# Optimization experiments

Hardware: AMD Instinct MI355X
Metric: run time of the kernel (lower is better)

Reference implementation:

```python
import jax, jax.numpy as jnp
import numpy as np

E = 8          # num_experts
K = 2          # top-k experts per token
CAP_RATIO = 1.05


def setup_inputs() -> dict:
    key = jax.random.key(0)
    ks = jax.random.split(key, 4)
    B, S, D, H = 2, 2048, 1024, 4096
    x = jax.random.normal(ks[0], (B, S, D), jnp.float32)
    Wg = jax.random.normal(ks[1], (E, D), jnp.float32) * 0.02
    W1 = jax.random.normal(ks[2], (E, D, H), jnp.float32) * 0.02
    b1 = jnp.zeros((E, H), jnp.float32)
    W2 = jax.random.normal(ks[3], (E, H, D), jnp.float32) * 0.02
    b2 = jnp.zeros((E, D), jnp.float32)
    return {"x": x, "Wg": Wg, "W1": W1, "b1": b1, "W2": W2, "b2": b2}


def reference(x, Wg, W1, b1, W2, b2):
    # Eval-mode SparseMoE forward (no router noise, no aux-loss metrics).
    B, S, D = x.shape
    T = B * S
    xf = x.reshape(T, D)

    # --- router: softmax gates + top-k ---
    gates = jax.nn.softmax(xf @ Wg.T, axis=-1)          # [T, E]
    topw, topi = jax.lax.top_k(gates, K)                # [T, K]

    # --- capacity-limited dispatch (slot-major order, matching torch loop) ---
    C = int(round(K * T * CAP_RATIO / E))               # buffer capacity per expert
    e_ord = topi.T.reshape(-1)                          # [K*T] expert id per assignment
    tok_ord = jnp.tile(jnp.arange(T), K)                # [K*T] token id per assignment
    oh = jax.nn.one_hot(e_ord, E, dtype=jnp.int32)      # [K*T, E]
    cnt = jnp.take_along_axis(jnp.cumsum(oh, 0) - oh, e_ord[:, None], 1)[:, 0]
    within = cnt < C                                    # first C arrivals per expert accepted
    pos = jnp.where(within, cnt, C)                     # dropped tokens -> dummy slot C

    # scatter accepted tokens into per-expert buffers [E, C+1, D]
    x_disp = xf[tok_ord]
    buf = jnp.zeros((E, C + 1, D), xf.dtype).at[e_ord, pos].add(x_disp)[:, :C]

    # --- grouped expert MLP (Linear -> exact GELU -> Linear) ---
    h = jax.nn.gelu(jnp.einsum('ecd,edh->ech', buf, W1) + b1[:, None, :],
                    approximate=False)
    y = jnp.einsum('ech,ehd->ecd', h, W2) + b2[:, None, :]  # [E, C, D]

    # --- gather back and weighted combine ---
    y_ord = y[e_ord, jnp.minimum(pos, C - 1)] * within[:, None].astype(y.dtype)
    y_tk = y_ord.reshape(K, T, D).transpose(1, 0, 2)     # [T, K, D]
    cw = topw * within.reshape(K, T).T.astype(topw.dtype)
    out = jnp.einsum('tk,tkd->td', cw, y_tk)
    return out.reshape(B, S, D)
```

## Files before the change

### kernel.cpp

```cpp
#include <hip/hip_runtime.h>

typedef __attribute__((ext_vector_type(8))) __bf16 bf16x8;
typedef __attribute__((ext_vector_type(4))) float f32x4;

constexpr int T  = 4096;
constexpr int Dm = 1024;
constexpr int Hm = 4096;
constexpr int NE = 8;
constexpr int CAP = 1075;
constexpr int CP  = 1152;

static __device__ __forceinline__ unsigned short f2bf(float f) {
  unsigned int u = __float_as_uint(f);
  u += 0x7FFFu + ((u >> 16) & 1u);
  return (unsigned short)(u >> 16);
}
static __device__ __forceinline__ float bf2f(unsigned short u) {
  return __uint_as_float(((unsigned int)u) << 16);
}

static __device__ __forceinline__ void gload_lds16(const void* g, void* l) {
  __builtin_amdgcn_global_load_lds(
      (const __attribute__((address_space(1))) void*)g,
      (__attribute__((address_space(3))) void*)l, 16, 0, 0);
}


static __device__ __forceinline__ void transpose_body(
    float (*tile)[33], const float* __restrict__ W, unsigned short* __restrict__ Wt,
    int Kd, int N, int e, int n0, int k0) {
  const float* src = W + ((long long)e * Kd + k0) * N + n0;
  const int tid = threadIdx.x;
  const int r = tid >> 3;
  const int c4 = (tid & 7) * 4;
#pragma unroll
  for (int hh = 0; hh < 2; ++hh) {
    float4 v = *(const float4*)(src + (long long)(r + 32 * hh) * N + c4);
    tile[r + 32 * hh][c4] = v.x; tile[r + 32 * hh][c4 + 1] = v.y;
    tile[r + 32 * hh][c4 + 2] = v.z; tile[r + 32 * hh][c4 + 3] = v.w;
  }
  __syncthreads();
  const int n = tid >> 4;
  const int k4 = (tid & 15) * 4;
  unsigned short* dst = Wt + ((long long)e * N + n0) * Kd + k0;
#pragma unroll
  for (int hh = 0; hh < 2; ++hh) {
    int nn = n + 16 * hh;
    ushort4 o;
    o.x = f2bf(tile[k4][nn]);     o.y = f2bf(tile[k4 + 1][nn]);
    o.z = f2bf(tile[k4 + 2][nn]); o.w = f2bf(tile[k4 + 3][nn]);
    *(ushort4*)(dst + (long long)nn * Kd + k4) = o;
  }
}

static __device__ __forceinline__ void router_body(
    const float* __restrict__ x, const float* __restrict__ Wg,
    int* __restrict__ topi, float* __restrict__ topw, int blk) {
  int t = blk * 4 + (threadIdx.x >> 6);
  int lane = threadIdx.x & 63;
  const float* xr = x + (size_t)t * Dm;
  float acc[NE];
#pragma unroll
  for (int e = 0; e < NE; ++e) acc[e] = 0.f;
  for (int i = lane * 4; i < Dm; i += 256) {
    float4 xv = *(const float4*)(xr + i);
#pragma unroll
    for (int e = 0; e < NE; ++e) {
      float4 wv = *(const float4*)(Wg + e * Dm + i);
      acc[e] += xv.x * wv.x + xv.y * wv.y + xv.z * wv.z + xv.w * wv.w;
    }
  }
#pragma unroll
  for (int off = 32; off > 0; off >>= 1) {
#pragma unroll
    for (int e = 0; e < NE; ++e) acc[e] += __shfl_xor(acc[e], off, 64);
  }
  if (lane == 0) {
    float mx = acc[0];
#pragma unroll
    for (int e = 1; e < NE; ++e) mx = fmaxf(mx, acc[e]);
    float g[NE];
    float s = 0.f;
#pragma unroll
    for (int e = 0; e < NE; ++e) { g[e] = expf(acc[e] - mx); s += g[e]; }
    int i0 = 0; float v0 = g[0];
#pragma unroll
    for (int e = 1; e < NE; ++e) if (g[e] > v0) { v0 = g[e]; i0 = e; }
    int i1 = -1; float v1 = -1e30f;
#pragma unroll
    for (int e = 0; e < NE; ++e) {
      if (e == i0) continue;
      if (g[e] > v1) { v1 = g[e]; i1 = e; }
    }
    float inv = 1.f / s;
    topi[t * 2] = i0; topi[t * 2 + 1] = i1;
    topw[t * 2] = v0 * inv; topw[t * 2 + 1] = v1 * inv;
  }
}

static __device__ __forceinline__ void stage_tile(
    unsigned short* Al, unsigned short* Bl,
    const unsigned short* __restrict__ Ab, const unsigned short* __restrict__ Btb,
    int Kd, int kb, int wid, int srow, int sslot) {
#pragma unroll
  for (int j = 0; j < 4; ++j) {
    const int c = wid * 4 + j;
    const long long rowg = 8 * c + srow;
    gload_lds16(Ab  + rowg * Kd + kb + sslot * 8, &Al[c * 512]);
    gload_lds16(Btb + rowg * Kd + kb + sslot * 8, &Bl[c * 512]);
  }
}

static __device__ __forceinline__ void compute_tile(
    const unsigned short* Al, const unsigned short* Bl,
    int wr, int wc, int l15, int khi, int swz, f32x4 (&acc)[4][4]) {
#pragma unroll
  for (int kk = 0; kk < 2; ++kk) {
    bf16x8 af[4], bfv[4];
#pragma unroll
    for (int m = 0; m < 4; ++m)
      af[m] = *(const bf16x8*)&Al[(wr + m * 16 + l15) * 64 + (((kk * 4 + khi) ^ swz) << 3)];
#pragma unroll
    for (int n = 0; n < 4; ++n)
      bfv[n] = *(const bf16x8*)&Bl[(wc + n * 16 + l15) * 64 + (((kk * 4 + khi) ^ swz) << 3)];
#pragma unroll
    for (int m = 0; m < 4; ++m)
#pragma unroll
      for (int n = 0; n < 4; ++n)
        acc[m][n] = __builtin_amdgcn_mfma_f32_16x16x32_bf16(af[m], bfv[n], acc[m][n], 0, 0, 0);
  }
}

static __device__ __forceinline__ void gemm_mainloop_db(
    char* smem, const unsigned short* __restrict__ Ab,
    const unsigned short* __restrict__ Btb, int Kd, f32x4 (&acc)[4][4]) {
  unsigned short* A0 = (unsigned short*)smem;
  unsigned short* B0 = (unsigned short*)(smem + 16384);
  unsigned short* A1 = (unsigned short*)(smem + 32768);
  unsigned short* B1 = (unsigned short*)(smem + 49152);
  const int tid = threadIdx.x;
  const int lane = tid & 63;
  const int wid = tid >> 6;
  const int wr = (wid >> 1) * 64;
  const int wc = (wid & 1) * 64;
  const int l15 = lane & 15;
  const int khi = lane >> 4;
  const int swz = lane & 7;
  const int srow = lane >> 3;
  const int sslot = (lane & 7) ^ srow;

  const int nK = Kd >> 6;
  stage_tile(A0, B0, Ab, Btb, Kd, 0, wid, srow, sslot);
  int cur = 0;
  for (int kt = 0; kt < nK - 1; ++kt) {
    unsigned short* An = cur ? A0 : A1;
    unsigned short* Bn = cur ? B0 : B1;
    stage_tile(An, Bn, Ab, Btb, Kd, (kt + 1) << 6, wid, srow, sslot);
    asm volatile("s_waitcnt vmcnt(8)" ::: "memory");
    __builtin_amdgcn_s_barrier();
    unsigned short* Ac = cur ? A1 : A0;
    unsigned short* Bc = cur ? B1 : B0;
    compute_tile(Ac, Bc, wr, wc, l15, khi, swz, acc);
    __builtin_amdgcn_s_barrier();
    cur ^= 1;
  }
  asm volatile("s_waitcnt vmcnt(0)" ::: "memory");
  __builtin_amdgcn_s_barrier();
  compute_tile(cur ? A1 : A0, cur ? B1 : B0, wr, wc, l15, khi, swz, acc);
}


__global__ __launch_bounds__(256) void fused_pre_kernel(
    const float* __restrict__ x, const float* __restrict__ Wg,
    int* __restrict__ topi, float* __restrict__ topw,
    const float* __restrict__ W1, unsigned short* __restrict__ W1t,
    const float* __restrict__ W2, unsigned short* __restrict__ W2t,
    int nR, int nT2) {
  __shared__ __align__(16) float tile[64][33];
  const int bid = blockIdx.x;
  if (bid < nR) {
    router_body(x, Wg, topi, topw, bid);
  } else if (bid < nR + nT2) {
    int tb = bid - nR;
    int nb = tb % (Dm / 32);
    int rest = tb / (Dm / 32);
    int kb = rest % (Hm / 64);
    int e = rest / (Hm / 64);
    transpose_body(tile, W2, W2t, Hm, Dm, e, nb * 32, kb * 64);
  } else {
    int tb = bid - nR - nT2;
    int nb = tb % (Hm / 32);
    int rest = tb / (Hm / 32);
    int kb = rest % (Dm / 64);
    int e = rest / (Dm / 64);
    transpose_body(tile, W1, W1t, Dm, Hm, e, nb * 32, kb * 64);
  }
}

__global__ __launch_bounds__(1024) void dispatch_scan_kernel(
    const int* __restrict__ topi, int* __restrict__ pos, int* __restrict__ within,
    int* __restrict__ cnt) {
  __shared__ unsigned long long sc0[1024];
  __shared__ unsigned long long sc1[1024];
  const int tid = threadIdx.x;
  int myE[8];
  unsigned long long w0 = 0, w1 = 0;
#pragma unroll
  for (int j = 0; j < 8; ++j) {
    int a = tid * 8 + j;
    int k = a >> 12;
    int t = a & (T - 1);
    int e = topi[t * 2 + k];
    myE[j] = e;
    unsigned long long inc = 1ULL << (16 * (e & 3));
    if (e < 4) w0 += inc; else w1 += inc;
  }
  const unsigned long long l0 = w0, l1 = w1;
  sc0[tid] = w0; sc1[tid] = w1;
  __syncthreads();
  for (int off = 1; off < 1024; off <<= 1) {
    unsigned long long a0 = 0, a1 = 0;
    if (tid >= off) { a0 = sc0[tid - off]; a1 = sc1[tid - off]; }
    __syncthreads();
    w0 += a0; w1 += a1;
    sc0[tid] = w0; sc1[tid] = w1;
    __syncthreads();
  }
  if (tid == 1023) {
#pragma unroll
    for (int e = 0; e < 4; ++e) {
      cnt[e]     = (int)((w0 >> (16 * e)) & 0xFFFF);
      cnt[e + 4] = (int)((w1 >> (16 * e)) & 0xFFFF);
    }
  }
  unsigned long long e0 = w0 - l0, e1 = w1 - l1;
#pragma unroll
  for (int j = 0; j < 8; ++j) {
    int a = tid * 8 + j;
    int e = myE[j];
    int sh = 16 * (e & 3);
    int p;
    if (e < 4) { p = (int)((e0 >> sh) & 0xFFFF); e0 += 1ULL << sh; }
    else       { p = (int)((e1 >> sh) & 0xFFFF); e1 += 1ULL << sh; }
    pos[a] = p;
    within[a] = (p < CAP) ? 1 : 0;
  }
}

__global__ __launch_bounds__(256) void scatter_kernel(
    const float* __restrict__ x, const int* __restrict__ topi,
    const int* __restrict__ pos, const int* __restrict__ within,
    unsigned short* __restrict__ buf) {
  int a = blockIdx.x;
  if (!within[a]) return;
  int k = a >> 12, t = a & (T - 1);
  int e = topi[t * 2 + k];
  int p = pos[a];
  const float* src = x + (size_t)t * Dm;
  unsigned short* dst = buf + ((size_t)e * CP + p) * Dm;
  int i = threadIdx.x * 4;
  float4 v = *(const float4*)(src + i);
  ushort4 o;
  o.x = f2bf(v.x); o.y = f2bf(v.y); o.z = f2bf(v.z); o.w = f2bf(v.w);
  *(ushort4*)(dst + i) = o;
}

__global__ __launch_bounds__(256) void gemm1_kernel(
    const unsigned short* __restrict__ buf, const unsigned short* __restrict__ W1t,
    const float* __restrict__ b1, unsigned short* __restrict__ h,
    const int* __restrict__ cnt) {
  __shared__ __align__(16) char smem[65536];
  const int e = blockIdx.x & 7;
  const int q = blockIdx.x >> 3;
  const int mb = q % (CP / 128);
  const int nb = q / (CP / 128);
  const int ce = min(cnt[e], CAP);
  if (mb * 128 >= ce) return;

  f32x4 acc[4][4];
#pragma unroll
  for (int m = 0; m < 4; ++m)
#pragma unroll
    for (int n = 0; n < 4; ++n) acc[m][n] = (f32x4){0.f, 0.f, 0.f, 0.f};

  gemm_mainloop_db(smem,
                   buf + ((long long)e * CP + mb * 128) * Dm,
                   W1t + ((long long)e * Hm + nb * 128) * Dm, Dm, acc);

  const int lane = threadIdx.x & 63;
  const int wid = threadIdx.x >> 6;
  const int wr = (wid >> 1) * 64;
  const int wc = (wid & 1) * 64;
  const int l15 = lane & 15;
  const int crow = (lane >> 4) * 4;
  const float* bias = b1 + (size_t)e * Hm;
  unsigned short* H = h + (size_t)e * CP * Hm;
#pragma unroll
  for (int m = 0; m < 4; ++m) {
#pragma unroll
    for (int n = 0; n < 4; ++n) {
      const long long col = (long long)nb * 128 + wc + n * 16 + l15;
      const float bvv = bias[col];
#pragma unroll
      for (int j = 0; j < 4; ++j) {
        const long long row = (long long)mb * 128 + wr + m * 16 + crow + j;
        float v = acc[m][n][j] + bvv;
        v = 0.5f * v * (1.f + erff(v * 0.70710678118654752f));
        H[row * Hm + col] = f2bf(v);
      }
    }
  }
}

__global__ __launch_bounds__(256) void gemm2_kernel(
    const unsigned short* __restrict__ h, const unsigned short* __restrict__ W2t,
    const float* __restrict__ b2, unsigned short* __restrict__ y,
    const int* __restrict__ cnt) {
  __shared__ __align__(16) char smem[65536];
  const int e = blockIdx.x & 7;
  const int q = blockIdx.x >> 3;
  const int mb = q % (CP / 128);
  const int nb = q / (CP / 128);
  const int ce = min(cnt[e], CAP);
  if (mb * 128 >= ce) return;

  f32x4 acc[4][4];
#pragma unroll
  for (int m = 0; m < 4; ++m)
#pragma unroll
    for (int n = 0; n < 4; ++n) acc[m][n] = (f32x4){0.f, 0.f, 0.f, 0.f};

  gemm_mainloop_db(smem,
                   h + ((long long)e * CP + mb * 128) * Hm,
                   W2t + ((long long)e * Dm + nb * 128) * Hm, Hm, acc);

  const int lane = threadIdx.x & 63;
  const int wid = threadIdx.x >> 6;
  const int wr = (wid >> 1) * 64;
  const int wc = (wid & 1) * 64;
  const int l15 = lane & 15;
  const int crow = (lane >> 4) * 4;
  const float* bias = b2 + (size_t)e * Dm;
  unsigned short* Y = y + (size_t)e * CP * Dm;
#pragma unroll
  for (int m = 0; m < 4; ++m) {
#pragma unroll
    for (int n = 0; n < 4; ++n) {
      const long long col = (long long)nb * 128 + wc + n * 16 + l15;
      const float bvv = bias[col];
#pragma unroll
      for (int j = 0; j < 4; ++j) {
        const long long row = (long long)mb * 128 + wr + m * 16 + crow + j;
        Y[row * Dm + col] = f2bf(acc[m][n][j] + bvv);
      }
    }
  }
}

__global__ __launch_bounds__(256) void combine_kernel(
    const unsigned short* __restrict__ y, const int* __restrict__ topi,
    const float* __restrict__ topw, const int* __restrict__ pos,
    const int* __restrict__ within, float* __restrict__ out) {
  int t = blockIdx.x;
  int i = threadIdx.x * 4;
  float4 r = {0.f, 0.f, 0.f, 0.f};
#pragma unroll
  for (int k = 0; k < 2; ++k) {
    int a = k * T + t;
    if (within[a]) {
      int e = topi[t * 2 + k];
      int p = pos[a];
      float w = topw[t * 2 + k];
      const unsigned short* yr = y + ((size_t)e * CP + p) * Dm + i;
      ushort4 v = *(const ushort4*)yr;
      r.x += w * bf2f(v.x); r.y += w * bf2f(v.y);
      r.z += w * bf2f(v.z); r.w += w * bf2f(v.w);
    }
  }
  *(float4*)(out + (size_t)t * Dm + i) = r;
}

__global__ __launch_bounds__(256) void transpose_kernel(
    const float* __restrict__ W, unsigned short* __restrict__ Wt, int Kd, int N) {
  __shared__ __align__(16) float tile[64][33];
  transpose_body(tile, W, Wt, Kd, N, blockIdx.z, blockIdx.x * 32, blockIdx.y * 64);
}

extern "C" void kernel_launch(void* const* d_in, const int* in_sizes, int n_in,
                              void* d_out, int out_size, void* d_ws, size_t ws_size,
                              hipStream_t stream) {
  const float* x  = (const float*)d_in[0];
  const float* Wg = (const float*)d_in[1];
  const float* W1 = (const float*)d_in[2];
  const float* b1 = (const float*)d_in[3];
  const float* W2 = (const float*)d_in[4];
  const float* b2 = (const float*)d_in[5];
  float* out = (float*)d_out;

  char* ws = (char*)d_ws;
  const size_t sz_h   = (size_t)NE * CP * Hm * 2;
  const size_t sz_buf = (size_t)NE * CP * Dm * 2;
  const size_t sz_w   = (size_t)NE * Hm * Dm * 2;
  const size_t sz_small = (size_t)2 * T * 4 * 4 + 64;
  const size_t need_full = sz_h + sz_buf + 2 * sz_w + sz_small;

  unsigned short* h   = (unsigned short*)ws;
  unsigned short* buf = (unsigned short*)(ws + sz_h);
  unsigned short* y   = buf;
  unsigned short* W1t = (unsigned short*)(ws + sz_h + sz_buf);
  const bool full = (ws_size >= need_full);
  unsigned short* W2t = full ? (W1t + sz_w / 2) : W1t;
  char* smallp = ws + sz_h + sz_buf + (full ? 2 * sz_w : sz_w);
  int*   topi   = (int*)smallp;
  float* topw   = (float*)(topi + 2 * T);
  int*   pos    = (int*)(topw + 2 * T);
  int*   within = pos + 2 * T;
  int*   cnt    = within + 2 * T;

  const int nM = CP / 128;
  const int nR = T / 4;
  const int nT = (Hm / 32) * (Dm / 64) * NE;
  const int nGemm1 = NE * nM * (Hm / 128);
  const int nGemm2 = NE * nM * (Dm / 128);

  if (full) {
    fused_pre_kernel<<<nR + 2 * nT, 256, 0, stream>>>(
        x, Wg, topi, topw, W1, W1t, W2, W2t, nR, nT);
    dispatch_scan_kernel<<<1, 1024, 0, stream>>>(topi, pos, within, cnt);
    scatter_kernel<<<2 * T, 256, 0, stream>>>(x, topi, pos, within, buf);
    gemm1_kernel<<<nGemm1, 256, 0, stream>>>(buf, W1t, b1, h, cnt);
    gemm2_kernel<<<nGemm2, 256, 0, stream>>>(h, W2t, b2, y, cnt);
  } else {
    fused_pre_kernel<<<nR + nT, 256, 0, stream>>>(
        x, Wg, topi, topw, W1, W1t, W2, W2t, nR, 0);
    dispatch_scan_kernel<<<1, 1024, 0, stream>>>(topi, pos, within, cnt);
    scatter_kernel<<<2 * T, 256, 0, stream>>>(x, topi, pos, within, buf);
    gemm1_kernel<<<nGemm1, 256, 0, stream>>>(buf, W1t, b1, h, cnt);
    transpose_kernel<<<dim3(Dm / 32, Hm / 64, NE), 256, 0, stream>>>(W2, W2t, Hm, Dm);
    gemm2_kernel<<<nGemm2, 256, 0, stream>>>(h, W2t, b2, y, cnt);
  }

  combine_kernel<<<T, 256, 0, stream>>>(y, topi, topw, pos, within, out);
}
```

Before: 343.4 us.

## Replace double-buffered LDS GEMM mainloop with single-buffered loop for occupancy

Removes the ping-pong LDS double buffer in the shared GEMM mainloop and uses a single 32KB buffer with load, barrier, compute, barrier per k-step. Global and LDS address pointers and swizzle offsets are precomputed outside the loop. Halving LDS use per block lets more blocks be resident per CU, at the cost of losing intra-block overlap of global loads with MFMA compute.

```diff
diff --git a/kernel.cpp b/kernel.cpp
--- a/kernel.cpp
+++ b/kernel.cpp
@@ -98,46 +98,10 @@
   }
 }
 
-static __device__ __forceinline__ void stage_tile(
-    unsigned short* Al, unsigned short* Bl,
+static __device__ __forceinline__ void gemm_mainloop(
+    unsigned short* Alds, unsigned short* Blds,
     const unsigned short* __restrict__ Ab, const unsigned short* __restrict__ Btb,
-    int Kd, int kb, int wid, int srow, int sslot) {
-#pragma unroll
-  for (int j = 0; j < 4; ++j) {
-    const int c = wid * 4 + j;
-    const long long rowg = 8 * c + srow;
-    gload_lds16(Ab  + rowg * Kd + kb + sslot * 8, &Al[c * 512]);
-    gload_lds16(Btb + rowg * Kd + kb + sslot * 8, &Bl[c * 512]);
-  }
-}
-
-static __device__ __forceinline__ void compute_tile(
-    const unsigned short* Al, const unsigned short* Bl,
-    int wr, int wc, int l15, int khi, int swz, f32x4 (&acc)[4][4]) {
-#pragma unroll
-  for (int kk = 0; kk < 2; ++kk) {
-    bf16x8 af[4], bfv[4];
-#pragma unroll
-    for (int m = 0; m < 4; ++m)
-      af[m] = *(const bf16x8*)&Al[(wr + m * 16 + l15) * 64 + (((kk * 4 + khi) ^ swz) << 3)];
-#pragma unroll
-    for (int n = 0; n < 4; ++n)
-      bfv[n] = *(const bf16x8*)&Bl[(wc + n * 16 + l15) * 64 + (((kk * 4 + khi) ^ swz) << 3)];
-#pragma unroll
-    for (int m = 0; m < 4; ++m)
-#pragma unroll
-      for (int n = 0; n < 4; ++n)
-        acc[m][n] = __builtin_amdgcn_mfma_f32_16x16x32_bf16(af[m], bfv[n], acc[m][n], 0, 0, 0);
-  }
-}
-
-static __device__ __forceinline__ void gemm_mainloop_db(
-    char* smem, const unsigned short* __restrict__ Ab,
-    const unsigned short* __restrict__ Btb, int Kd, f32x4 (&acc)[4][4]) {
-  unsigned short* A0 = (unsigned short*)smem;
-  unsigned short* B0 = (unsigned short*)(smem + 16384);
-  unsigned short* A1 = (unsigned short*)(smem + 32768);
-  unsigned short* B1 = (unsigned short*)(smem + 49152);
+    int Kd, f32x4 (&acc)[4][4]) {
   const int tid = threadIdx.x;
   const int lane = tid & 63;
   const int wid = tid >> 6;
@@ -149,24 +113,52 @@
   const int srow = lane >> 3;
   const int sslot = (lane & 7) ^ srow;
 
+  const unsigned short* pa[4];
+  const unsigned short* pb[4];
+  unsigned short* la[4];
+  unsigned short* lb[4];
+#pragma unroll
+  for (int j = 0; j < 4; ++j) {
+    const int c = wid * 4 + j;
+    const long long rowg = 8 * c + srow;
+    pa[j] = Ab  + rowg * Kd + sslot * 8;
+    pb[j] = Btb + rowg * Kd + sslot * 8;
+    la[j] = &Alds[c * 512];
+    lb[j] = &Blds[c * 512];
+  }
+  int rowA[4], rowB[4];
+#pragma unroll
+  for (int m = 0; m < 4; ++m) rowA[m] = (wr + m * 16 + l15) * 64;
+#pragma unroll
+  for (int n = 0; n < 4; ++n) rowB[n] = (wc + n * 16 + l15) * 64;
+  const int off0 = (khi ^ swz) << 3;
+  const int off1 = ((4 + khi) ^ swz) << 3;
+
   const int nK = Kd >> 6;
-  stage_tile(A0, B0, Ab, Btb, Kd, 0, wid, srow, sslot);
-  int cur = 0;
-  for (int kt = 0; kt < nK - 1; ++kt) {
-    unsigned short* An = cur ? A0 : A1;
-    unsigned short* Bn = cur ? B0 : B1;
-    stage_tile(An, Bn, Ab, Btb, Kd, (kt + 1) << 6, wid, srow, sslot);
-    asm volatile("s_waitcnt vmcnt(8)" ::: "memory");
-    __builtin_amdgcn_s_barrier();
-    unsigned short* Ac = cur ? A1 : A0;
-    unsigned short* Bc = cur ? B1 : B0;
-    compute_tile(Ac, Bc, wr, wc, l15, khi, swz, acc);
-    __builtin_amdgcn_s_barrier();
-    cur ^= 1;
-  }
-  asm volatile("s_waitcnt vmcnt(0)" ::: "memory");
-  __builtin_amdgcn_s_barrier();
-  compute_tile(cur ? A1 : A0, cur ? B1 : B0, wr, wc, l15, khi, swz, acc);
+  for (int kt = 0; kt < nK; ++kt) {
+#pragma unroll
+    for (int j = 0; j < 4; ++j) {
+      gload_lds16(pa[j], la[j]);
+      gload_lds16(pb[j], lb[j]);
+      pa[j] += 64; pb[j] += 64;
+    }
+    __syncthreads();
+#pragma unroll
+    for (int kk = 0; kk < 2; ++kk) {
+      const int off = kk ? off1 : off0;
+      bf16x8 af[4], bfv[4];
+#pragma unroll
+      for (int m = 0; m < 4; ++m) af[m] = *(const bf16x8*)&Alds[rowA[m] + off];
+#pragma unroll
+      for (int n = 0; n < 4; ++n) bfv[n] = *(const bf16x8*)&Blds[rowB[n] + off];
+#pragma unroll
+      for (int m = 0; m < 4; ++m)
+#pragma unroll
+        for (int n = 0; n < 4; ++n)
+          acc[m][n] = __builtin_amdgcn_mfma_f32_16x16x32_bf16(af[m], bfv[n], acc[m][n], 0, 0, 0);
+    }
+    __syncthreads();
+  }
 }
 
 
@@ -269,7 +261,8 @@
     const unsigned short* __restrict__ buf, const unsigned short* __restrict__ W1t,
     const float* __restrict__ b1, unsigned short* __restrict__ h,
     const int* __restrict__ cnt) {
-  __shared__ __align__(16) char smem[65536];
+  __shared__ __align__(16) unsigned short Alds[128 * 64];
+  __shared__ __align__(16) unsigned short Blds[128 * 64];
   const int e = blockIdx.x & 7;
   const int q = blockIdx.x >> 3;
   const int mb = q % (CP / 128);
@@ -283,9 +276,9 @@
 #pragma unroll
     for (int n = 0; n < 4; ++n) acc[m][n] = (f32x4){0.f, 0.f, 0.f, 0.f};
 
-  gemm_mainloop_db(smem,
-                   buf + ((long long)e * CP + mb * 128) * Dm,
-                   W1t + ((long long)e * Hm + nb * 128) * Dm, Dm, acc);
+  gemm_mainloop(Alds, Blds,
+                buf + ((long long)e * CP + mb * 128) * Dm,
+                W1t + ((long long)e * Hm + nb * 128) * Dm, Dm, acc);
 
   const int lane = threadIdx.x & 63;
   const int wid = threadIdx.x >> 6;
@@ -316,7 +309,8 @@
     const unsigned short* __restrict__ h, const unsigned short* __restrict__ W2t,
     const float* __restrict__ b2, unsigned short* __restrict__ y,
     const int* __restrict__ cnt) {
-  __shared__ __align__(16) char smem[65536];
+  __shared__ __align__(16) unsigned short Alds[128 * 64];
+  __shared__ __align__(16) unsigned short Blds[128 * 64];
   const int e = blockIdx.x & 7;
   const int q = blockIdx.x >> 3;
   const int mb = q % (CP / 128);
@@ -330,9 +324,9 @@
 #pragma unroll
     for (int n = 0; n < 4; ++n) acc[m][n] = (f32x4){0.f, 0.f, 0.f, 0.f};
 
-  gemm_mainloop_db(smem,
-                   h + ((long long)e * CP + mb * 128) * Hm,
-                   W2t + ((long long)e * Dm + nb * 128) * Hm, Hm, acc);
+  gemm_mainloop(Alds, Blds,
+                h + ((long long)e * CP + mb * 128) * Hm,
+                W2t + ((long long)e * Dm + nb * 128) * Hm, Hm, acc);
 
   const int lane = threadIdx.x & 63;
   const int wid = threadIdx.x >> 6;
```

After: 391.2 us. +13.9%, slower.
